# Performance work log

Hardware: AMD Instinct MI355X
Metric: run time of the kernel (lower is better)

Reference implementation:

```python
import jax, jax.numpy as jnp
import numpy as np

B, C, H, W = 8, 256, 96, 96
SH = SW = 8            # down_scale window
NHEADS = 8
HD = C // NHEADS       # 32
SCALE = HD ** -0.5


def setup_inputs() -> dict:
    key = jax.random.key(0)
    ks = jax.random.split(key, 9)
    s = 0.02
    return {
        "x": jax.random.normal(ks[0], (B, C, H, W), jnp.float32),
        "Wq": jax.random.normal(ks[1], (C, C), jnp.float32) * s,
        "Wkv": jax.random.normal(ks[2], (2 * C, C), jnp.float32) * s,
        "pool_w": jax.random.normal(ks[3], (C, C, SH, SW), jnp.float32) * s,
        "pool_b": jax.random.normal(ks[4], (C,), jnp.float32) * s,
        "rpe_w": jax.random.normal(ks[5], (C, 1, 3, 3), jnp.float32) * s,
        "rpe_b": jax.random.normal(ks[6], (C,), jnp.float32) * s,
        "proj_w": jax.random.normal(ks[7], (C, C), jnp.float32) * s,
        "proj_b": jax.random.normal(ks[8], (C,), jnp.float32) * s,
    }


def reference(x, Wq, Wkv, pool_w, pool_b, rpe_w, rpe_b, proj_w, proj_b):
    b, c, h, w = x.shape
    nHw, nWw = h // SH, w // SW
    L = nHw * nWw            # number of windows per image
    N = b * L                # total windows
    Q = SH * SW              # queries per window

    # partition (torch unfold with kernel=stride=window) -> [N, SH, SW, C]
    xw = x.reshape(b, c, nHw, SH, nWw, SW).transpose(0, 2, 4, 3, 5, 1)
    xw = xw.reshape(N, SH, SW, c)

    # sub-window pooling: full-window conv == weighted sum over window -> [B, L, C]
    pool_x = (jnp.einsum('nijc,ocij->no', xw, pool_w) + pool_b).reshape(b, L, c)

    # Q projection (no bias): [N, Q, nh, hd] -> [N, nh, Q, hd]
    q = (xw.reshape(N, Q, c) @ Wq.T).reshape(N, Q, NHEADS, HD).transpose(0, 2, 1, 3)
    q = q * SCALE

    # KV projection on pooled tokens (no bias): k, v [B, nh, L, hd]
    kv = (pool_x @ Wkv.T).reshape(b, L, 2, NHEADS, HD)
    k = kv[:, :, 0].transpose(0, 2, 1, 3)
    v = kv[:, :, 1].transpose(0, 2, 1, 3)
    # original tiles pool_x cat-style: window n uses KV of batch (n % B).
    # reshape q to groups g of size B: n = g*B + bb  -> [L, B, nh, Q, hd]
    qg = q.reshape(L, b, NHEADS, Q, HD)
    attn = jnp.einsum('gbhqd,bhkd->gbhqk', qg, k)       # [L, B, nh, Q, L]
    attn = jax.nn.softmax(attn, axis=-1)
    out = jnp.einsum('gbhqk,bhkd->gbhqd', attn, v)      # [L, B, nh, Q, hd]

    # faithful raw reshape: [N, nh, Q, hd] -> (N, Q, nh, hd) -> (B, C, H, W)
    out = out.reshape(N, NHEADS, Q, HD).transpose(0, 2, 1, 3).reshape(b, c, h, w)

    # depthwise 3x3 RPE on original x
    rpe = jax.lax.conv_general_dilated(
        x, rpe_w, window_strides=(1, 1), padding='SAME',
        feature_group_count=c,
        dimension_numbers=('NCHW', 'OIHW', 'NCHW')) + rpe_b[None, :, None, None]

    out = out + rpe
    y = out.reshape(b, -1, c) @ proj_w.T + proj_b       # [B, H*W, C]
    return y
```

## Files before the change

### kernel.cpp

```cpp
#include <hip/hip_runtime.h>
#include <math.h>

#define CB 8
#define CC 256
#define CH 96
#define CWD 96
#define CL 144
#define CN 1152
#define CQ 64
#define NHEADS 8
#define HD 32
#define HWSZ (CH*CWD)
#define QSCALE 0.17677669529663687f

typedef __attribute__((ext_vector_type(4))) float  f32x4;
typedef __attribute__((ext_vector_type(4))) short  s16x4;
typedef __attribute__((ext_vector_type(8))) short  s16x8;
typedef __attribute__((ext_vector_type(8))) __bf16 bf16x8;

static __device__ __forceinline__ short f2b(float f) {
  union { float f; unsigned u; } v; v.f = f;
  unsigned r = (v.u + 0x7fffu + ((v.u >> 16) & 1u)) >> 16;
  return (short)r;
}

static __device__ __forceinline__ bf16x8 pack8(float4 lo, float4 hi) {
  s16x8 p;
  p[0] = f2b(lo.x); p[1] = f2b(lo.y); p[2] = f2b(lo.z); p[3] = f2b(lo.w);
  p[4] = f2b(hi.x); p[5] = f2b(hi.y); p[6] = f2b(hi.z); p[7] = f2b(hi.w);
  return __builtin_bit_cast(bf16x8, p);
}

__global__ __launch_bounds__(256) void k_cvt(const float* __restrict__ s,
                                             short* __restrict__ d, int n8) {
  int i = blockIdx.x * 256 + threadIdx.x;
  if (i >= n8) return;
  const float4* p = (const float4*)s + (size_t)i * 2;
  float4 a = p[0], b = p[1];
  s16x8 o;
  o[0] = f2b(a.x); o[1] = f2b(a.y); o[2] = f2b(a.z); o[3] = f2b(a.w);
  o[4] = f2b(b.x); o[5] = f2b(b.y); o[6] = f2b(b.z); o[7] = f2b(b.w);
  *(s16x8*)(d + (size_t)i * 8) = o;
}

__global__ __launch_bounds__(256) void k_pool(const float* __restrict__ x,
                                              const short* __restrict__ pwb,
                                              float* __restrict__ part) {
  const int t = threadIdx.x, lane = t & 63, w = t >> 6;
  const int col = lane & 15, quad = lane >> 4;
  const int mb = blockIdx.x, nh = blockIdx.y, ks = blockIdx.z;
  const int wdx = mb * 64 + w * 16 + col;
  const int b = wdx / CL, l = wdx - b * CL;
  const int wh = l / 12, ww = l - wh * 12;
  const size_t xbase = (size_t)b * CC * HWSZ + wh * 8 * CWD + ww * 8;
  const int col0 = nh * 128;

  f32x4 acc[8] = {};

  for (int kc = 0; kc < 64; ++kc) {
    const int c = ks * 32 + (kc >> 1);
    const int i = (kc & 1) * 4 + quad;
    const float* ap = x + xbase + (size_t)c * HWSZ + i * CWD;
    float4 lo = *(const float4*)ap, hi = *(const float4*)(ap + 4);
    bf16x8 af = pack8(lo, hi);
    const int kg = ks * 2048 + kc * 32 + quad * 8;
#pragma unroll
    for (int ot = 0; ot < 8; ++ot) {
      s16x8 rb = *(const s16x8*)(pwb + (size_t)(col0 + ot * 16 + col) * 16384 + kg);
      acc[ot] = __builtin_amdgcn_mfma_f32_16x16x32_bf16(
          af, __builtin_bit_cast(bf16x8, rb), acc[ot], 0, 0, 0);
    }
  }

  float* pp = part + ((size_t)ks * CN + mb * 64 + w * 16) * CC + col0;
#pragma unroll
  for (int ot = 0; ot < 8; ++ot)
#pragma unroll
    for (int r = 0; r < 4; ++r)
      pp[(quad * 4 + r) * CC + ot * 16 + col] = acc[ot][r];
}

__global__ __launch_bounds__(256) void k_poolred(const float* __restrict__ part,
                                                 const float* __restrict__ pbv,
                                                 float* __restrict__ pxr) {
  int base = (blockIdx.x * 256 + threadIdx.x) * 4;
  int m = base & 255;
  float4 s = *(const float4*)&pbv[m];
#pragma unroll
  for (int ss = 0; ss < 8; ++ss) {
    float4 p = *(const float4*)&part[(size_t)ss * (CN * CC) + base];
    s.x += p.x; s.y += p.y; s.z += p.z; s.w += p.w;
  }
  *(float4*)&pxr[base] = s;
}

__global__ __launch_bounds__(256) void k_kv(const float* __restrict__ pxr,
                                            const float* __restrict__ wkv,
                                            float* __restrict__ kbuf,
                                            float* __restrict__ vbuf) {
  const int t = threadIdx.x, tx = t & 15, ty = t >> 4;
  const int row0 = blockIdx.x * 64;
  const int col0 = blockIdx.y * 64;
  __shared__ float As[16][68];
  __shared__ float Bs[16][68];
  float acc[4][4] = {};
  const int ml = t & 15, rB = t >> 4;

  for (int mc = 0; mc < 16; ++mc) {
#pragma unroll
    for (int u = 0; u < 4; ++u) {
      int r = rB + 16 * u;
      As[ml][r] = pxr[(row0 + r) * CC + mc * 16 + ml];
      Bs[ml][r] = wkv[(col0 + r) * CC + mc * 16 + ml];
    }
    __syncthreads();
#pragma unroll
    for (int kk = 0; kk < 16; ++kk) {
      float4 a4 = *(const float4*)&As[kk][ty * 4];
      float4 b4 = *(const float4*)&Bs[kk][tx * 4];
      float av[4] = {a4.x, a4.y, a4.z, a4.w};
      float bv[4] = {b4.x, b4.y, b4.z, b4.w};
#pragma unroll
      for (int ri = 0; ri < 4; ++ri)
#pragma unroll
        for (int cj = 0; cj < 4; ++cj) acc[ri][cj] += av[ri] * bv[cj];
    }
    __syncthreads();
  }

#pragma unroll
  for (int ri = 0; ri < 4; ++ri) {
    int row = row0 + ty * 4 + ri;
    int b = row / CL, l = row - b * CL;
    int j = col0 + tx * 4;
    int d = j & 31, h = (j >> 5) & 7, tkv = j >> 8;
    float* dst = (tkv ? vbuf : kbuf) + ((size_t)(b * NHEADS + h) * CL + l) * HD + d;
    *(float4*)dst = make_float4(acc[ri][0], acc[ri][1], acc[ri][2], acc[ri][3]);
  }
}

__global__ __launch_bounds__(256) void k_q(const float* __restrict__ x,
                                           const short* __restrict__ wqb,
                                           float* __restrict__ qout) {
  const int t = threadIdx.x, lane = t & 63, w = t >> 6;
  const int col = lane & 15, quad = lane >> 4;
  const int n = blockIdx.x;
  const int b = n / CL, l = n - b * CL;
  const int wh = l / 12, ww = l - wh * 12;
  const size_t xwin = (size_t)b * CC * HWSZ + wh * 8 * CWD + ww * 8;

  __shared__ short xq[64][264];
  {
    const int ci = t & 31, ii = t >> 5;
#pragma unroll
    for (int u = 0; u < 8; ++u) {
      const float* ap = x + xwin + (size_t)(ci + 32 * u) * HWSZ + ii * CWD;
      float4 lo = *(const float4*)ap, hi = *(const float4*)(ap + 4);
      float vals[8] = {lo.x, lo.y, lo.z, lo.w, hi.x, hi.y, hi.z, hi.w};
#pragma unroll
      for (int j = 0; j < 8; ++j) xq[ii * 8 + j][ci + 32 * u] = f2b(vals[j]);
    }
  }
  __syncthreads();

  f32x4 acc[4][4] = {};
  for (int kc = 0; kc < 8; ++kc) {
    bf16x8 af[4];
#pragma unroll
    for (int cht = 0; cht < 4; ++cht) {
      s16x8 r = *(const s16x8*)(wqb + (size_t)(w * 64 + cht * 16 + col) * CC + kc * 32 + quad * 8);
      af[cht] = __builtin_bit_cast(bf16x8, r);
    }
#pragma unroll
    for (int qt = 0; qt < 4; ++qt) {
      s16x8 rb = *(const s16x8*)&xq[qt * 16 + col][kc * 32 + quad * 8];
      bf16x8 bfv = __builtin_bit_cast(bf16x8, rb);
#pragma unroll
      for (int cht = 0; cht < 4; ++cht)
        acc[cht][qt] = __builtin_amdgcn_mfma_f32_16x16x32_bf16(af[cht], bfv, acc[cht][qt], 0, 0, 0);
    }
  }

  float* op = qout + (size_t)n * CQ * CC;
#pragma unroll
  for (int qt = 0; qt < 4; ++qt)
#pragma unroll
    for (int cht = 0; cht < 4; ++cht) {
      f32x4 v = acc[cht][qt];
      *(float4*)&op[(qt * 16 + col) * CC + w * 64 + cht * 16 + quad * 4] =
          make_float4(v[0] * QSCALE, v[1] * QSCALE, v[2] * QSCALE, v[3] * QSCALE);
    }
}

__global__ __launch_bounds__(256) void k_attn(const float* __restrict__ kbuf,
                                              const float* __restrict__ vbuf,
                                              float* __restrict__ S) {
  const int t = threadIdx.x;
  const int wv = t >> 6, lane = t & 63;
  const int col = lane & 15, quad = lane >> 4;
  const int task = blockIdx.x * 4 + wv;
  const int n = task >> 3, h = task & 7;
  const int bb = n & 7;

  const float* kh = kbuf + (size_t)(bb * NHEADS + h) * CL * HD;
  const float* vh = vbuf + (size_t)(bb * NHEADS + h) * CL * HD;
  float* Sn = S + (size_t)n * (CQ * CC) + h * HD;

  bf16x8 ka[9];
#pragma unroll
  for (int lt = 0; lt < 9; ++lt) {
    const float* kr = kh + (lt * 16 + col) * HD + quad * 8;
    ka[lt] = pack8(*(const float4*)kr, *(const float4*)(kr + 4));
  }

  s16x4 vt[2][9];
#pragma unroll
  for (int dt = 0; dt < 2; ++dt)
#pragma unroll
    for (int lc = 0; lc < 9; ++lc) {
      s16x4 p;
#pragma unroll
      for (int j = 0; j < 4; ++j)
        p[j] = f2b(vh[(lc * 16 + quad * 4 + j) * HD + dt * 16 + col]);
      vt[dt][lc] = p;
    }

  const f32x4 zero = {0.f, 0.f, 0.f, 0.f};

#pragma unroll
  for (int qt = 0; qt < 4; ++qt) {
    const float* qr = Sn + (size_t)(qt * 16 + col) * CC + quad * 8;
    bf16x8 qb = pack8(*(const float4*)qr, *(const float4*)(qr + 4));

    f32x4 s[9];
#pragma unroll
    for (int lt = 0; lt < 9; ++lt)
      s[lt] = __builtin_amdgcn_mfma_f32_16x16x32_bf16(ka[lt], qb, zero, 0, 0, 0);

    float mx = s[0][0];
#pragma unroll
    for (int lt = 0; lt < 9; ++lt)
#pragma unroll
      for (int r = 0; r < 4; ++r) mx = fmaxf(mx, s[lt][r]);
    mx = fmaxf(mx, __shfl_xor(mx, 16, 64));
    mx = fmaxf(mx, __shfl_xor(mx, 32, 64));

    float sum = 0.f;
    s16x4 pb[9];
#pragma unroll
    for (int lt = 0; lt < 9; ++lt) {
      s16x4 pp;
#pragma unroll
      for (int r = 0; r < 4; ++r) {
        float e = __expf(s[lt][r] - mx);
        sum += e;
        pp[r] = f2b(e);
      }
      pb[lt] = pp;
    }
    sum += __shfl_xor(sum, 16, 64);
    sum += __shfl_xor(sum, 32, 64);
    const float inv = 1.0f / sum;

    f32x4 o0 = zero, o1 = zero;
#pragma unroll
    for (int lc = 0; lc < 9; ++lc) {
      o0 = __builtin_amdgcn_mfma_f32_16x16x16bf16_1k(vt[0][lc], pb[lc], o0, 0, 0, 0);
      o1 = __builtin_amdgcn_mfma_f32_16x16x16bf16_1k(vt[1][lc], pb[lc], o1, 0, 0, 0);
    }

    float* orow = Sn + (size_t)(qt * 16 + col) * CC;
    *(float4*)&orow[quad * 4] =
        make_float4(o0[0] * inv, o0[1] * inv, o0[2] * inv, o0[3] * inv);
    *(float4*)&orow[16 + quad * 4] =
        make_float4(o1[0] * inv, o1[1] * inv, o1[2] * inv, o1[3] * inv);
  }
}

__global__ __launch_bounds__(256) void k_rpe(const float* __restrict__ x,
                                             const float* __restrict__ rw,
                                             const float* __restrict__ rb,
                                             float* __restrict__ S) {
  const int bc = blockIdx.x;
  const int c = bc & 255;
  const int t = threadIdx.x;
  __shared__ float xs[HWSZ];
  const float* xp = x + (size_t)bc * HWSZ;
  float* sp = S + (size_t)bc * HWSZ;
#pragma unroll
  for (int u = 0; u < 36; ++u) xs[t + 256 * u] = xp[t + 256 * u];
  float w9[9];
#pragma unroll
  for (int k = 0; k < 9; ++k) w9[k] = rw[c * 9 + k];
  const float bias = rb[c];
  __syncthreads();
  for (int u = 0; u < 36; ++u) {
    int idx = t + 256 * u;
    int hh = idx / 96, ww = idx - hh * 96;
    float s = bias;
#pragma unroll
    for (int di = 0; di < 3; ++di) {
      int h2 = hh + di - 1;
#pragma unroll
      for (int dj = 0; dj < 3; ++dj) {
        int w2 = ww + dj - 1;
        if ((unsigned)h2 < 96u && (unsigned)w2 < 96u)
          s += xs[h2 * 96 + w2] * w9[di * 3 + dj];
      }
    }
    sp[idx] += s;
  }
}

__global__ __launch_bounds__(256) void k_proj(const short* __restrict__ pjwb,
                                              const float* __restrict__ pjb,
                                              float* __restrict__ S) {
  const int t = threadIdx.x, lane = t & 63, w = t >> 6;
  const int col = lane & 15, quad = lane >> 4;
  const size_t row0 = (size_t)blockIdx.x * 64;

  __shared__ short Sl[64][264];
  const float* Sp = S + row0 * CC;
#pragma unroll
  for (int u = 0; u < 16; ++u) {
    int idx = u * 1024 + t * 4;
    float4 v = *(const float4*)&Sp[idx];
    s16x4 pv;
    pv[0] = f2b(v.x); pv[1] = f2b(v.y); pv[2] = f2b(v.z); pv[3] = f2b(v.w);
    *(s16x4*)&Sl[idx >> 8][idx & 255] = pv;
  }
  __syncthreads();

  f32x4 acc[4][4] = {};
  for (int kc = 0; kc < 8; ++kc) {
    bf16x8 bfr[4];
#pragma unroll
    for (int ot = 0; ot < 4; ++ot) {
      s16x8 r = *(const s16x8*)(pjwb + (size_t)(w * 64 + ot * 16 + col) * CC + kc * 32 + quad * 8);
      bfr[ot] = __builtin_bit_cast(bf16x8, r);
    }
#pragma unroll
    for (int mt = 0; mt < 4; ++mt) {
      s16x8 ra = *(const s16x8*)&Sl[mt * 16 + col][kc * 32 + quad * 8];
      bf16x8 af = __builtin_bit_cast(bf16x8, ra);
#pragma unroll
      for (int ot = 0; ot < 4; ++ot)
        acc[mt][ot] = __builtin_amdgcn_mfma_f32_16x16x32_bf16(af, bfr[ot], acc[mt][ot], 0, 0, 0);
    }
  }

  float bias[4];
#pragma unroll
  for (int ot = 0; ot < 4; ++ot) bias[ot] = pjb[w * 64 + ot * 16 + col];
  float* Sw = S + row0 * CC;
#pragma unroll
  for (int mt = 0; mt < 4; ++mt)
#pragma unroll
    for (int ot = 0; ot < 4; ++ot)
#pragma unroll
      for (int r = 0; r < 4; ++r)
        Sw[(mt * 16 + quad * 4 + r) * CC + w * 64 + ot * 16 + col] = acc[mt][ot][r] + bias[ot];
}

extern "C" void kernel_launch(void* const* d_in, const int* in_sizes, int n_in,
                              void* d_out, int out_size, void* d_ws, size_t ws_size,
                              hipStream_t stream) {
  const float* x    = (const float*)d_in[0];
  const float* wq   = (const float*)d_in[1];
  const float* wkv  = (const float*)d_in[2];
  const float* pw   = (const float*)d_in[3];
  const float* pbv  = (const float*)d_in[4];
  const float* rw   = (const float*)d_in[5];
  const float* rb   = (const float*)d_in[6];
  const float* pjw  = (const float*)d_in[7];
  const float* pjb  = (const float*)d_in[8];
  float* out = (float*)d_out;
  float* ws  = (float*)d_ws;

  float* part = ws;
  float* pxr  = part + 8 * CN * CC;
  float* kbuf = pxr + CN * CC;
  float* vbuf = kbuf + CB * NHEADS * CL * HD;
  short* pwb  = (short*)(vbuf + CB * NHEADS * CL * HD);
  short* wqb  = pwb + 4194304;
  short* pjwb = wqb + 65536;

  k_cvt    <<<2048, 256, 0, stream>>>(pw,  pwb,  524288);
  k_cvt    <<<32,   256, 0, stream>>>(wq,  wqb,  8192);
  k_cvt    <<<32,   256, 0, stream>>>(pjw, pjwb, 8192);

  k_pool   <<<dim3(18, 2, 8), 256, 0, stream>>>(x, pwb, part);
  k_poolred<<<288,            256, 0, stream>>>(part, pbv, pxr);
  k_kv     <<<dim3(18, 8),    256, 0, stream>>>(pxr, wkv, kbuf, vbuf);
  k_q      <<<CN,             256, 0, stream>>>(x, wqb, out);
  k_attn   <<<2304,           256, 0, stream>>>(kbuf, vbuf, out);
  k_rpe    <<<CB * CC,        256, 0, stream>>>(x, rw, rb, out);
  k_proj   <<<1152,           256, 0, stream>>>(pjwb, pjb, out);
}
```

Measured before the change: 512.9 us.

## Reorder pool weights into K-chunk-major layout and split pooling K across more slices

Converts the pooling conv weights into a chunked layout where each 32-wide K chunk for all outputs is contiguous, so the MFMA B-operand loads in the pooling kernel read compact, coalesced blocks instead of rows strided by 16384 elements. The split-K factor rises from 8 to 32 slices, giving 1152 blocks instead of 288 for better occupancy, at the cost of a larger partial-sum buffer and reduction. The partial buffer is placed in the output tensor, which is overwritten later, to avoid needing extra workspace.

Result: faster. 442.0 us (-13.8%).

```diff
diff --git a/kernel.cpp b/kernel.cpp
--- a/kernel.cpp
+++ b/kernel.cpp
@@ -12,6 +12,7 @@
 #define HD 32
 #define HWSZ (CH*CWD)
 #define QSCALE 0.17677669529663687f
+#define NSLICE 32
 
 typedef __attribute__((ext_vector_type(4))) float  f32x4;
 typedef __attribute__((ext_vector_type(4))) short  s16x4;
@@ -43,8 +44,24 @@
   *(s16x8*)(d + (size_t)i * 8) = o;
 }
 
+__global__ __launch_bounds__(256) void k_cvtp(const float* __restrict__ pw,
+                                              short* __restrict__ pw2) {
+  int g = blockIdx.x * 256 + threadIdx.x;
+  int kk8 = (g & 3) * 8;
+  int o   = (g >> 2) & 255;
+  int kc  = (g >> 10) & 15;
+  int ks  = g >> 14;
+  int kglob = ks * 512 + kc * 32 + kk8;
+  const float* src = pw + (size_t)o * 16384 + kglob;
+  float4 a = *(const float4*)src, b = *(const float4*)(src + 4);
+  s16x8 oo;
+  oo[0] = f2b(a.x); oo[1] = f2b(a.y); oo[2] = f2b(a.z); oo[3] = f2b(a.w);
+  oo[4] = f2b(b.x); oo[5] = f2b(b.y); oo[6] = f2b(b.z); oo[7] = f2b(b.w);
+  *(s16x8*)(pw2 + (size_t)g * 8) = oo;
+}
+
 __global__ __launch_bounds__(256) void k_pool(const float* __restrict__ x,
-                                              const short* __restrict__ pwb,
+                                              const short* __restrict__ pw2,
                                               float* __restrict__ part) {
   const int t = threadIdx.x, lane = t & 63, w = t >> 6;
   const int col = lane & 15, quad = lane >> 4;
@@ -53,26 +70,25 @@
   const int b = wdx / CL, l = wdx - b * CL;
   const int wh = l / 12, ww = l - wh * 12;
   const size_t xbase = (size_t)b * CC * HWSZ + wh * 8 * CWD + ww * 8;
-  const int col0 = nh * 128;
 
   f32x4 acc[8] = {};
 
-  for (int kc = 0; kc < 64; ++kc) {
-    const int c = ks * 32 + (kc >> 1);
+#pragma unroll 4
+  for (int kc = 0; kc < 16; ++kc) {
+    const int c = ks * 8 + (kc >> 1);
     const int i = (kc & 1) * 4 + quad;
     const float* ap = x + xbase + (size_t)c * HWSZ + i * CWD;
-    float4 lo = *(const float4*)ap, hi = *(const float4*)(ap + 4);
-    bf16x8 af = pack8(lo, hi);
-    const int kg = ks * 2048 + kc * 32 + quad * 8;
+    bf16x8 af = pack8(*(const float4*)ap, *(const float4*)(ap + 4));
+    const short* bk = pw2 + ((size_t)(ks * 16 + kc) * 256 + nh * 128) * 32;
 #pragma unroll
     for (int ot = 0; ot < 8; ++ot) {
-      s16x8 rb = *(const s16x8*)(pwb + (size_t)(col0 + ot * 16 + col) * 16384 + kg);
+      s16x8 rb = *(const s16x8*)(bk + (ot * 16 + col) * 32 + quad * 8);
       acc[ot] = __builtin_amdgcn_mfma_f32_16x16x32_bf16(
           af, __builtin_bit_cast(bf16x8, rb), acc[ot], 0, 0, 0);
     }
   }
 
-  float* pp = part + ((size_t)ks * CN + mb * 64 + w * 16) * CC + col0;
+  float* pp = part + ((size_t)ks * CN + mb * 64 + w * 16) * CC + nh * 128;
 #pragma unroll
   for (int ot = 0; ot < 8; ++ot)
 #pragma unroll
@@ -87,7 +103,7 @@
   int m = base & 255;
   float4 s = *(const float4*)&pbv[m];
 #pragma unroll
-  for (int ss = 0; ss < 8; ++ss) {
+  for (int ss = 0; ss < NSLICE; ++ss) {
     float4 p = *(const float4*)&part[(size_t)ss * (CN * CC) + base];
     s.x += p.x; s.y += p.y; s.z += p.z; s.w += p.w;
   }
@@ -377,19 +393,20 @@
   float* out = (float*)d_out;
   float* ws  = (float*)d_ws;
 
-  float* part = ws;
-  float* pxr  = part + 8 * CN * CC;
+  float* pxr  = ws;
   float* kbuf = pxr + CN * CC;
   float* vbuf = kbuf + CB * NHEADS * CL * HD;
-  short* pwb  = (short*)(vbuf + CB * NHEADS * CL * HD);
-  short* wqb  = pwb + 4194304;
+  short* pw2  = (short*)(vbuf + CB * NHEADS * CL * HD);
+  short* wqb  = pw2 + 4194304;
   short* pjwb = wqb + 65536;
 
-  k_cvt    <<<2048, 256, 0, stream>>>(pw,  pwb,  524288);
+  float* part = out;
+
+  k_cvtp   <<<2048, 256, 0, stream>>>(pw, pw2);
   k_cvt    <<<32,   256, 0, stream>>>(wq,  wqb,  8192);
   k_cvt    <<<32,   256, 0, stream>>>(pjw, pjwb, 8192);
 
-  k_pool   <<<dim3(18, 2, 8), 256, 0, stream>>>(x, pwb, part);
+  k_pool   <<<dim3(18, 2, NSLICE), 256, 0, stream>>>(x, pw2, part);
   k_poolred<<<288,            256, 0, stream>>>(part, pbv, pxr);
   k_kv     <<<dim3(18, 8),    256, 0, stream>>>(pxr, wkv, kbuf, vbuf);
   k_q      <<<CN,             256, 0, stream>>>(x, wqb, out);
```
